# Kernel tuning notes

Measured on AMD Instinct MI355X. Metric: run time of the kernel, lower is better.

The kernel has to match this reference:

```python
import jax, jax.numpy as jnp
import numpy as np

N = 100000   # nodes
E = 1200000  # edges
D = 64       # input_features == hidden_features
L = 3        # num_layers
EPS = 1e-5   # BatchNorm1d eps
SLOPE = 0.2  # LeakyReLU negative slope


def setup_inputs() -> dict:
    key = jax.random.key(0)
    k_x, k_e, k_w = jax.random.split(key, 3)
    x = jax.random.normal(k_x, (N, D), dtype=jnp.float32)
    edge_index = jax.random.randint(k_e, (2, E), 0, N, dtype=jnp.int32)
    # Glorot-ish linear weights per layer, stacked [L, D, D]; bias zeros.
    Ws = jax.random.normal(k_w, (L, D, D), dtype=jnp.float32) / np.float32(np.sqrt(D))
    bs = jnp.zeros((L, D), dtype=jnp.float32)
    # BatchNorm affine params (training-mode batch statistics are used).
    gammas = jnp.ones((L, D), dtype=jnp.float32)
    betas = jnp.zeros((L, D), dtype=jnp.float32)
    return {"x": x, "edge_index": edge_index, "Ws": Ws, "bs": bs,
            "gammas": gammas, "betas": betas}


def reference(x, edge_index, Ws, bs, gammas, betas):
    src, dst = edge_index[0], edge_index[1]
    # GCN symmetric normalization with self-loops: deg = in-degree + 1
    deg = jax.ops.segment_sum(jnp.ones((E,), x.dtype), dst, num_segments=N) + 1.0
    dinv = jax.lax.rsqrt(deg)
    enorm = (dinv[src] * dinv[dst])[:, None]  # [E,1] edge norm
    snorm = (dinv * dinv)[:, None]            # [N,1] self-loop norm
    for l in range(L):
        xw = x @ Ws[l]                                        # [N,D]
        agg = (jax.ops.segment_sum(xw[src] * enorm, dst, num_segments=N)
               + xw * snorm + bs[l])                          # GCNConv output
        h = jnp.where(agg > 0, agg, SLOPE * agg)              # LeakyReLU(0.2)
        mu = h.mean(axis=0)
        var = h.var(axis=0)                                   # biased var (PyTorch BN)
        x = gammas[l] * (h - mu) * jax.lax.rsqrt(var + EPS) + betas[l]
    return x
```

## Files before the change

kernel.cpp:

```cpp
#include <hip/hip_runtime.h>

#define D 64
#define SLOPE 0.2f
#define BN_EPS 1e-5f
#define BSHIFT 9
#define CHUNK 7168

static __device__ __forceinline__ unsigned pk_bf16(float fx, float fy) {
    unsigned bx = __float_as_uint(fx);
    unsigned by = __float_as_uint(fy);
    bx = (bx + 0x7fffu + ((bx >> 16) & 1u)) >> 16;
    by = (by + 0x7fffu + ((by >> 16) & 1u)) & 0xffff0000u;
    return bx | by;
}
static __device__ __forceinline__ float bf_lo(unsigned u) { return __uint_as_float(u << 16); }
static __device__ __forceinline__ float bf_hi(unsigned u) { return __uint_as_float(u & 0xffff0000u); }

__global__ __launch_bounds__(256) void k_hist(const int* __restrict__ dst,
                                              int* __restrict__ bcnt, int E, int NB) {
    __shared__ int hist[256];
    for (int i = threadIdx.x; i < NB; i += 256) hist[i] = 0;
    __syncthreads();
    for (int e = blockIdx.x * 256 + threadIdx.x; e < E; e += gridDim.x * 256)
        atomicAdd(&hist[dst[e] >> BSHIFT], 1);
    __syncthreads();
    for (int i = threadIdx.x; i < NB; i += 256)
        if (hist[i]) atomicAdd(&bcnt[i], hist[i]);
}

__global__ __launch_bounds__(256) void k_bscan(const int* __restrict__ bcnt,
                                               int* __restrict__ bbase, int* __restrict__ pcur,
                                               int* __restrict__ rp, int NB, int E, int N) {
    __shared__ int l[256];
    const int t = threadIdx.x;
    const int v = (t < NB) ? bcnt[t] : 0;
    l[t] = v;
    __syncthreads();
    for (int off = 1; off < 256; off <<= 1) {
        int x = l[t];
        if (t >= off) x += l[t - off];
        __syncthreads();
        l[t] = x;
        __syncthreads();
    }
    if (t < NB) {
        const int excl = l[t] - v;
        bbase[t] = excl;
        pcur[t]  = excl;
    }
    if (t == 0) { bbase[NB] = E; rp[N] = E; }
}

__global__ __launch_bounds__(256) void k_part(const int* __restrict__ src,
                                              const int* __restrict__ dst,
                                              int* __restrict__ pcur,
                                              uint2* __restrict__ arena,
                                              int E, int NB, int nchunks) {
    __shared__ uint2 stage[CHUNK];
    __shared__ int hist[256], lofs[256], gbase[256];

    for (int chunk = blockIdx.x; chunk < nchunks; chunk += gridDim.x) {
        const int e0 = chunk * CHUNK;
        const int cn = min(CHUNK, E - e0);

        for (int i = threadIdx.x; i < NB; i += 256) hist[i] = 0;
        __syncthreads();
        for (int i = threadIdx.x; i < cn; i += 256)
            atomicAdd(&hist[dst[e0 + i] >> BSHIFT], 1);
        __syncthreads();

        {
            const int t = threadIdx.x;
            const int v = (t < NB) ? hist[t] : 0;
            l_scan:
            lofs[t] = v;
            __syncthreads();
            for (int off = 1; off < 256; off <<= 1) {
                int x = lofs[t];
                if (t >= off) x += lofs[t - off];
                __syncthreads();
                lofs[t] = x;
                __syncthreads();
            }
            const int excl = lofs[t] - v;
            __syncthreads();
            lofs[t] = excl;
            if (t < NB && v > 0) gbase[t] = atomicAdd(&pcur[t], v);
            __syncthreads();
        }

        for (int i = threadIdx.x; i < cn; i += 256) {
            const int d = dst[e0 + i];
            const int s = src[e0 + i];
            const int b = d >> BSHIFT;
            const int p = atomicAdd(&lofs[b], 1);
            stage[p] = make_uint2((unsigned)s, (unsigned)d);
        }
        __syncthreads();

        for (int i = threadIdx.x; i < cn; i += 256) {
            const uint2 u = stage[i];
            const int b = (int)(u.y >> BSHIFT);
            const int startb = lofs[b] - hist[b];
            arena[gbase[b] + (i - startb)] = u;
        }
        __syncthreads();
    }
}

__global__ __launch_bounds__(512) void k_build(const uint2* __restrict__ arena,
                                               const int* __restrict__ bbase,
                                               int* __restrict__ rp, int* __restrict__ colbuf,
                                               float* __restrict__ dinv, int N) {
    const int b = blockIdx.x;
    const int nbase = b << BSHIFT;
    const int nlocal = min(1 << BSHIFT, N - nbase);
    const int abeg = bbase[b];
    const int aend = bbase[b + 1];
    __shared__ int ncnt[512], sc[512], lcur[512];
    const int t = threadIdx.x;

    ncnt[t] = 0;
    __syncthreads();
    for (int i = abeg + t; i < aend; i += 512)
        atomicAdd(&ncnt[(int)(arena[i].y) - nbase], 1);
    __syncthreads();

    const int v = ncnt[t];
    sc[t] = v;
    __syncthreads();
    for (int off = 1; off < 512; off <<= 1) {
        int x = sc[t];
        if (t >= off) x += sc[t - off];
        __syncthreads();
        sc[t] = x;
        __syncthreads();
    }
    const int excl = sc[t] - v;
    lcur[t] = excl;
    if (t < nlocal) {
        rp[nbase + t]   = abeg + excl;
        dinv[nbase + t] = rsqrtf((float)v + 1.0f);
    }
    __syncthreads();

    for (int i = abeg + t; i < aend; i += 512) {
        const uint2 u = arena[i];
        const int ln = (int)u.y - nbase;
        const int p = atomicAdd(&lcur[ln], 1);
        colbuf[abeg + p] = (int)u.x;
    }
}

__global__ void k_prep(const float* __restrict__ W, const float* __restrict__ stats,
                       const float* __restrict__ gamma, const float* __restrict__ beta,
                       float* __restrict__ Wp, float* __restrict__ bvec,
                       float invN, int affine) {
    __shared__ float scs[D], shs[D];
    const int t = threadIdx.x;
    if (t < D) {
        float sc = 1.0f, sh = 0.0f;
        if (affine) {
            const float mu  = stats[t] * invN;
            const float var = stats[D + t] * invN - mu * mu;
            sc = gamma[t] * rsqrtf(var + BN_EPS);
            sh = beta[t] - mu * sc;
        }
        scs[t] = sc; shs[t] = sh;
    }
    __syncthreads();
    for (int i = t; i < D * D; i += blockDim.x)
        Wp[i] = scs[i >> 6] * W[i];
    if (t < D) {
        float s = 0.0f;
#pragma unroll
        for (int k = 0; k < D; ++k) s += shs[k] * W[k * D + t];
        bvec[t] = s;
    }
}

__global__ __launch_bounds__(256) void k_gemm(const float* __restrict__ x,
                                              const float* __restrict__ Wp,
                                              const float* __restrict__ bvec,
                                              const float* __restrict__ dinv,
                                              unsigned* __restrict__ ybf, int N) {
    const int lane = threadIdx.x & 63;
    const int wib  = threadIdx.x >> 6;
    float Wreg[D];
#pragma unroll
    for (int k = 0; k < D; ++k) Wreg[k] = Wp[k * D + lane];
    const float bv = bvec[lane];
    const int stride = gridDim.x * 4;

    for (int row = __builtin_amdgcn_readfirstlane(blockIdx.x * 4 + wib); row < N; row += stride) {
        const float4* xr = (const float4*)(x + (size_t)row * D);
        float acc = 0.0f;
#pragma unroll
        for (int k4 = 0; k4 < 16; ++k4) {
            const float4 xv = xr[k4];
            acc = fmaf(xv.x, Wreg[4 * k4 + 0], acc);
            acc = fmaf(xv.y, Wreg[4 * k4 + 1], acc);
            acc = fmaf(xv.z, Wreg[4 * k4 + 2], acc);
            acc = fmaf(xv.w, Wreg[4 * k4 + 3], acc);
        }
        const float r  = (acc + bv) * dinv[row];
        const float rn = __shfl_down(r, 1, 64);
        if (!(lane & 1))
            ybf[(size_t)row * 32 + (lane >> 1)] = pk_bf16(r, rn);
    }
}

__global__ __launch_bounds__(256) void k_pull(const int* __restrict__ rp,
                                              const int* __restrict__ colbuf,
                                              const uint2* __restrict__ ybf2,
                                              const float* __restrict__ dinv,
                                              const float* __restrict__ bvecin,
                                              float* __restrict__ h,
                                              float* __restrict__ stats, int N) {
    const int lane = threadIdx.x & 63;
    const int sl   = lane & 15;
    const int qw   = lane >> 4;
    const int wib  = threadIdx.x >> 6;
    const float4 bb = *(const float4*)&bvecin[4 * sl];
    const float* bp = &bb.x;
    float s1[4] = {0.f, 0.f, 0.f, 0.f}, s2[4] = {0.f, 0.f, 0.f, 0.f};

    const int wid = blockIdx.x * 4 + wib;
    const int wstride = gridDim.x * 4;

    for (int n0 = wid * 2; n0 < N; n0 += wstride * 2) {
        const int n1 = n0 + 1;
        const bool has1 = n1 < N;
        const int2 r01 = *(const int2*)&rp[n0];
        const int start = r01.x;
        const int mid   = r01.y;
        const int end   = has1 ? rp[n0 + 2] : r01.y;

        float a[4][4], ba[4][4];
#pragma unroll
        for (int c = 0; c < 4; ++c)
#pragma unroll
            for (int f = 0; f < 4; ++f) { a[c][f] = 0.f; ba[c][f] = 0.f; }

        if (qw == 0) {
            const uint2 u = ybf2[(size_t)n0 * 16 + sl];
            a[0][0] += bf_lo(u.x); a[0][1] += bf_hi(u.x);
            a[0][2] += bf_lo(u.y); a[0][3] += bf_hi(u.y);
        } else if (qw == 1 && has1) {
            const uint2 u = ybf2[(size_t)n1 * 16 + sl];
            const float f0 = bf_lo(u.x), f1 = bf_hi(u.x), f2 = bf_lo(u.y), f3 = bf_hi(u.y);
            a[0][0] += f0; a[0][1] += f1; a[0][2] += f2; a[0][3] += f3;
            ba[0][0] += f0; ba[0][1] += f1; ba[0][2] += f2; ba[0][3] += f3;
        }

        for (int j = start; j < end; j += 64) {
            const int rem = end - j;
            const int cn  = rem < 64 ? rem : 64;
            const int ci  = (lane < cn) ? colbuf[j + lane] : 0;
            for (int s = 0; 16 * s < cn; ++s) {
#pragma unroll
                for (int c = 0; c < 4; ++c) {
                    const int e   = 16 * s + 4 * c + qw;
                    const int idx = __shfl(ci, e, 64);
                    uint2 u = ybf2[(size_t)idx * 16 + sl];
                    const bool val = e < cn;
                    const bool is1 = (j + e) >= mid;
                    u.x = val ? u.x : 0u;
                    u.y = val ? u.y : 0u;
                    const float f0 = bf_lo(u.x), f1 = bf_hi(u.x);
                    const float f2 = bf_lo(u.y), f3 = bf_hi(u.y);
                    a[c][0] += f0; a[c][1] += f1; a[c][2] += f2; a[c][3] += f3;
                    ba[c][0] += is1 ? f0 : 0.f;
                    ba[c][1] += is1 ? f1 : 0.f;
                    ba[c][2] += is1 ? f2 : 0.f;
                    ba[c][3] += is1 ? f3 : 0.f;
                }
            }
        }

        float vA[4], vB[4];
#pragma unroll
        for (int f = 0; f < 4; ++f) {
            vA[f] = (a[0][f] + a[1][f]) + (a[2][f] + a[3][f]);
            vA[f] += __shfl_xor(vA[f], 16, 64);
            vA[f] += __shfl_xor(vA[f], 32, 64);
            vB[f] = (ba[0][f] + ba[1][f]) + (ba[2][f] + ba[3][f]);
            vB[f] += __shfl_xor(vB[f], 16, 64);
            vB[f] += __shfl_xor(vB[f], 32, 64);
        }

        if (qw == 0) {
            const float di = dinv[n0];
            float4 hv; float* hp = &hv.x;
#pragma unroll
            for (int f = 0; f < 4; ++f) {
                float t = fmaf(di, vA[f] - vB[f], bp[f]);
                t = t > 0.f ? t : SLOPE * t;
                hp[f] = t; s1[f] += t; s2[f] += t * t;
            }
            *(float4*)&h[(size_t)n0 * D + 4 * sl] = hv;
        } else if (qw == 1 && has1) {
            const float di = dinv[n1];
            float4 hv; float* hp = &hv.x;
#pragma unroll
            for (int f = 0; f < 4; ++f) {
                float t = fmaf(di, vB[f], bp[f]);
                t = t > 0.f ? t : SLOPE * t;
                hp[f] = t; s1[f] += t; s2[f] += t * t;
            }
            *(float4*)&h[(size_t)n1 * D + 4 * sl] = hv;
        }
    }

    __shared__ float s1d[8][16][4], s2d[8][16][4];
    if (qw < 2) {
#pragma unroll
        for (int f = 0; f < 4; ++f) {
            s1d[wib * 2 + qw][sl][f] = s1[f];
            s2d[wib * 2 + qw][sl][f] = s2[f];
        }
    }
    __syncthreads();
    const int tid = threadIdx.x;
    if (tid < 64) {
        const int ssl = tid >> 2, f = tid & 3;
        float A = 0.f, B = 0.f;
#pragma unroll
        for (int g = 0; g < 8; ++g) { A += s1d[g][ssl][f]; B += s2d[g][ssl][f]; }
        atomicAdd(&stats[tid], A);
        atomicAdd(&stats[64 + tid], B);
    }
}

__global__ void k_normalize(const float* __restrict__ h, const float* __restrict__ stats,
                            const float* __restrict__ gamma, const float* __restrict__ beta,
                            float* __restrict__ out, float invN, int total) {
    const int col = threadIdx.x & 63;
    const float mu  = stats[col] * invN;
    const float var = stats[64 + col] * invN - mu * mu;
    const float sc  = gamma[col] * rsqrtf(var + BN_EPS);
    const float sh  = beta[col] - mu * sc;
    for (int i = blockIdx.x * blockDim.x + threadIdx.x; i < total; i += gridDim.x * blockDim.x)
        out[i] = fmaf(sc, h[i], sh);
}

extern "C" void kernel_launch(void* const* d_in, const int* in_sizes, int n_in,
                              void* d_out, int out_size, void* d_ws, size_t ws_size,
                              hipStream_t stream) {
    const float* x0     = (const float*)d_in[0];
    const int*   ei     = (const int*)d_in[1];
    const float* Ws     = (const float*)d_in[2];
    const float* bs     = (const float*)d_in[3];
    const float* gammas = (const float*)d_in[4];
    const float* betas  = (const float*)d_in[5];

    const int N = in_sizes[0] / D;
    const int E = in_sizes[1] / 2;
    const int L = in_sizes[2] / (D * D);
    const int NB = (N + (1 << BSHIFT) - 1) >> BSHIFT;
    const int nchunks = (E + CHUNK - 1) / CHUNK;

    const int* srcp = ei;
    const int* dstp = ei + E;

    char* wsb = (char*)d_ws;
    size_t o = 0;
    auto alloc = [&](size_t elems) { size_t r = o; o += (elems + 255) & ~(size_t)255; return r; };
    const size_t o_bcnt  = alloc(256);
    const size_t o_stats = alloc((size_t)L * 128);
    const size_t zero_end = o;
    const size_t o_bbase = alloc(257);
    const size_t o_pcur  = alloc(256);
    const size_t o_rp    = alloc((size_t)N + 1);
    const size_t o_dinv  = alloc((size_t)N);
    const size_t o_arena = alloc((size_t)E * 2);
    const size_t o_col   = alloc((size_t)E);
    const size_t o_wp    = alloc((size_t)D * D);
    const size_t o_bvec  = alloc((size_t)D);
    const size_t o_y     = alloc((size_t)N * 32);
    const size_t o_h     = alloc((size_t)N * D);

    int*      bcnt  = (int*)(wsb + o_bcnt * 4);
    float*    stats = (float*)(wsb + o_stats * 4);
    int*      bbase = (int*)(wsb + o_bbase * 4);
    int*      pcur  = (int*)(wsb + o_pcur * 4);
    int*      rp    = (int*)(wsb + o_rp * 4);
    float*    dinv  = (float*)(wsb + o_dinv * 4);
    uint2*    arena = (uint2*)(wsb + o_arena * 4);
    int*      col   = (int*)(wsb + o_col * 4);
    float*    Wp    = (float*)(wsb + o_wp * 4);
    float*    bvec  = (float*)(wsb + o_bvec * 4);
    unsigned* ybf   = (unsigned*)(wsb + o_y * 4);
    float*    h     = (float*)(wsb + o_h * 4);
    float*    out   = (float*)d_out;

    hipMemsetAsync(d_ws, 0, zero_end * 4, stream);

    k_hist<<<512, 256, 0, stream>>>(dstp, bcnt, E, NB);
    k_bscan<<<1, 256, 0, stream>>>(bcnt, bbase, pcur, rp, NB, E, N);
    k_part<<<nchunks, 256, 0, stream>>>(srcp, dstp, pcur, arena, E, NB, nchunks);
    k_build<<<NB, 512, 0, stream>>>(arena, bbase, rp, col, dinv, N);

    const float invN = 1.0f / (float)N;
    const float* xin = x0;
    for (int l = 0; l < L; ++l) {
        const float* Wl = Ws + (size_t)l * D * D;
        const float* bl = bs + (size_t)l * D;
        k_prep<<<1, 256, 0, stream>>>(Wl, stats + (size_t)(l ? l - 1 : 0) * 128,
                                      gammas + (size_t)(l ? l - 1 : 0) * D,
                                      betas + (size_t)(l ? l - 1 : 0) * D,
                                      Wp, bvec, invN, l > 0 ? 1 : 0);
        k_gemm<<<1024, 256, 0, stream>>>(xin, Wp, bvec, dinv, ybf, N);
        k_pull<<<2048, 256, 0, stream>>>(rp, col, (const uint2*)ybf, dinv, bl, h,
                                         stats + (size_t)l * 128, N);
        xin = h;
    }
    k_normalize<<<1024, 256, 0, stream>>>(h, stats + (size_t)(L - 1) * 128,
                                          gammas + (size_t)(L - 1) * D,
                                          betas + (size_t)(L - 1) * D, out, invN, N * D);
}
```

Baseline: 424.1 us.

## Pack CSR edges, pad rows to multiples of eight, fuse prep into gemm

Edges are packed into 32-bit words holding the local destination and the source, which halves arena traffic in the partition and build passes. CSR rows are padded to multiples of eight and filled with a dummy zero row, so the pull kernel can gather unconditionally with half-wave-per-node unrolled loads. The per-layer BN-folding prep kernel is merged into the GEMM, which saves a launch per layer. Normalization now uses float4 accesses. The packing caps sources below 2^23 and adds padding memory plus wasted gathers on the dummy row.

```diff
diff --git a/kernel.cpp b/kernel.cpp
--- a/kernel.cpp
+++ b/kernel.cpp
@@ -4,7 +4,8 @@
 #define SLOPE 0.2f
 #define BN_EPS 1e-5f
 #define BSHIFT 9
-#define CHUNK 7168
+#define BUCKET 512
+#define CHUNK 8192
 
 static __device__ __forceinline__ unsigned pk_bf16(float fx, float fy) {
     unsigned bx = __float_as_uint(fx);
@@ -17,20 +18,20 @@
 static __device__ __forceinline__ float bf_hi(unsigned u) { return __uint_as_float(u & 0xffff0000u); }
 
 __global__ __launch_bounds__(256) void k_hist(const int* __restrict__ dst,
-                                              int* __restrict__ bcnt, int E, int NB) {
+                                              int* __restrict__ bcnt, int E) {
     __shared__ int hist[256];
-    for (int i = threadIdx.x; i < NB; i += 256) hist[i] = 0;
+    hist[threadIdx.x] = 0;
     __syncthreads();
     for (int e = blockIdx.x * 256 + threadIdx.x; e < E; e += gridDim.x * 256)
         atomicAdd(&hist[dst[e] >> BSHIFT], 1);
     __syncthreads();
-    for (int i = threadIdx.x; i < NB; i += 256)
-        if (hist[i]) atomicAdd(&bcnt[i], hist[i]);
+    const int v = hist[threadIdx.x];
+    if (v) atomicAdd(&bcnt[threadIdx.x], v);
 }
 
 __global__ __launch_bounds__(256) void k_bscan(const int* __restrict__ bcnt,
                                                int* __restrict__ bbase, int* __restrict__ pcur,
-                                               int* __restrict__ rp, int NB, int E, int N) {
+                                               unsigned* __restrict__ ybf, int NB, int E, int N) {
     __shared__ int l[256];
     const int t = threadIdx.x;
     const int v = (t < NB) ? bcnt[t] : 0;
@@ -43,91 +44,79 @@
         l[t] = x;
         __syncthreads();
     }
-    if (t < NB) {
-        const int excl = l[t] - v;
-        bbase[t] = excl;
-        pcur[t]  = excl;
-    }
-    if (t == 0) { bbase[NB] = E; rp[N] = E; }
+    const int excl = l[t] - v;
+    if (t < NB) { bbase[t] = excl; pcur[t] = excl; }
+    if (t == 0) bbase[NB] = E;
+    if (t < 32) ybf[(size_t)N * 32 + t] = 0u;
 }
 
 __global__ __launch_bounds__(256) void k_part(const int* __restrict__ src,
                                               const int* __restrict__ dst,
                                               int* __restrict__ pcur,
-                                              uint2* __restrict__ arena,
-                                              int E, int NB, int nchunks) {
-    __shared__ uint2 stage[CHUNK];
+                                              unsigned* __restrict__ arena, int E) {
+    __shared__ unsigned stage[CHUNK];
+    __shared__ unsigned char bktb[CHUNK];
     __shared__ int hist[256], lofs[256], gbase[256];
-
-    for (int chunk = blockIdx.x; chunk < nchunks; chunk += gridDim.x) {
-        const int e0 = chunk * CHUNK;
-        const int cn = min(CHUNK, E - e0);
-
-        for (int i = threadIdx.x; i < NB; i += 256) hist[i] = 0;
-        __syncthreads();
-        for (int i = threadIdx.x; i < cn; i += 256)
-            atomicAdd(&hist[dst[e0 + i] >> BSHIFT], 1);
-        __syncthreads();
-
-        {
-            const int t = threadIdx.x;
-            const int v = (t < NB) ? hist[t] : 0;
-            l_scan:
-            lofs[t] = v;
-            __syncthreads();
-            for (int off = 1; off < 256; off <<= 1) {
-                int x = lofs[t];
-                if (t >= off) x += lofs[t - off];
-                __syncthreads();
-                lofs[t] = x;
-                __syncthreads();
-            }
-            const int excl = lofs[t] - v;
-            __syncthreads();
-            lofs[t] = excl;
-            if (t < NB && v > 0) gbase[t] = atomicAdd(&pcur[t], v);
-            __syncthreads();
-        }
-
-        for (int i = threadIdx.x; i < cn; i += 256) {
-            const int d = dst[e0 + i];
-            const int s = src[e0 + i];
-            const int b = d >> BSHIFT;
-            const int p = atomicAdd(&lofs[b], 1);
-            stage[p] = make_uint2((unsigned)s, (unsigned)d);
-        }
-        __syncthreads();
-
-        for (int i = threadIdx.x; i < cn; i += 256) {
-            const uint2 u = stage[i];
-            const int b = (int)(u.y >> BSHIFT);
-            const int startb = lofs[b] - hist[b];
-            arena[gbase[b] + (i - startb)] = u;
-        }
-        __syncthreads();
-    }
-}
-
-__global__ __launch_bounds__(512) void k_build(const uint2* __restrict__ arena,
+    const int t = threadIdx.x;
+    const int e0 = blockIdx.x * CHUNK;
+    const int cn = min(CHUNK, E - e0);
+
+    hist[t] = 0;
+    __syncthreads();
+    for (int i = t; i < cn; i += 256)
+        atomicAdd(&hist[dst[e0 + i] >> BSHIFT], 1);
+    __syncthreads();
+    const int v = hist[t];
+    lofs[t] = v;
+    __syncthreads();
+    for (int off = 1; off < 256; off <<= 1) {
+        int x = lofs[t];
+        if (t >= off) x += lofs[t - off];
+        __syncthreads();
+        lofs[t] = x;
+        __syncthreads();
+    }
+    const int excl = lofs[t] - v;
+    __syncthreads();
+    lofs[t] = excl;
+    if (v > 0) gbase[t] = atomicAdd(&pcur[t], v);
+    __syncthreads();
+    for (int i = t; i < cn; i += 256) {
+        const int dd = dst[e0 + i];
+        const int b  = dd >> BSHIFT;
+        const int p  = atomicAdd(&lofs[b], 1);
+        stage[p] = ((unsigned)(dd & (BUCKET - 1)) << 23) | (unsigned)src[e0 + i];
+        bktb[p]  = (unsigned char)b;
+    }
+    __syncthreads();
+    for (int i = t; i < cn; i += 256) {
+        const int b = bktb[i];
+        const int startb = lofs[b] - hist[b];
+        arena[gbase[b] + (i - startb)] = stage[i];
+    }
+}
+
+__global__ __launch_bounds__(512) void k_build(const unsigned* __restrict__ arena,
                                                const int* __restrict__ bbase,
-                                               int* __restrict__ rp, int* __restrict__ colbuf,
-                                               float* __restrict__ dinv, int N) {
-    const int b = blockIdx.x;
-    const int nbase = b << BSHIFT;
-    const int nlocal = min(1 << BSHIFT, N - nbase);
-    const int abeg = bbase[b];
-    const int aend = bbase[b + 1];
+                                               int* __restrict__ rp, int* __restrict__ pcnt,
+                                               int* __restrict__ colbuf, float* __restrict__ dinv,
+                                               int N) {
     __shared__ int ncnt[512], sc[512], lcur[512];
     const int t = threadIdx.x;
+    const int nbase  = blockIdx.x << BSHIFT;
+    const int nlocal = min(BUCKET, N - nbase);
+    const int abeg = bbase[blockIdx.x];
+    const int aend = bbase[blockIdx.x + 1];
+    const int pbase = abeg + 7 * nbase;
 
     ncnt[t] = 0;
     __syncthreads();
     for (int i = abeg + t; i < aend; i += 512)
-        atomicAdd(&ncnt[(int)(arena[i].y) - nbase], 1);
-    __syncthreads();
-
+        atomicAdd(&ncnt[arena[i] >> 23], 1);
+    __syncthreads();
     const int v = ncnt[t];
-    sc[t] = v;
+    const int p = (v + 7) & ~7;
+    sc[t] = p;
     __syncthreads();
     for (int off = 1; off < 512; off <<= 1) {
         int x = sc[t];
@@ -136,65 +125,59 @@
         sc[t] = x;
         __syncthreads();
     }
-    const int excl = sc[t] - v;
-    lcur[t] = excl;
+    const int excl = sc[t] - p;
+    lcur[t] = pbase + excl;
     if (t < nlocal) {
-        rp[nbase + t]   = abeg + excl;
+        rp[nbase + t]   = pbase + excl;
+        pcnt[nbase + t] = p;
         dinv[nbase + t] = rsqrtf((float)v + 1.0f);
     }
     __syncthreads();
-
     for (int i = abeg + t; i < aend; i += 512) {
-        const uint2 u = arena[i];
-        const int ln = (int)u.y - nbase;
-        const int p = atomicAdd(&lcur[ln], 1);
-        colbuf[abeg + p] = (int)u.x;
-    }
-}
-
-__global__ void k_prep(const float* __restrict__ W, const float* __restrict__ stats,
-                       const float* __restrict__ gamma, const float* __restrict__ beta,
-                       float* __restrict__ Wp, float* __restrict__ bvec,
-                       float invN, int affine) {
+        const unsigned u = arena[i];
+        const int pos = atomicAdd(&lcur[u >> 23], 1);
+        colbuf[pos] = (int)(u & 0x7FFFFFu);
+    }
+    if (t < nlocal)
+        for (int k = v; k < p; ++k) colbuf[pbase + excl + k] = N;
+}
+
+__global__ __launch_bounds__(256) void k_gemm(const float* __restrict__ x,
+                                              const float* __restrict__ W,
+                                              const float* __restrict__ stats,
+                                              const float* __restrict__ gamma,
+                                              const float* __restrict__ beta,
+                                              const float* __restrict__ dinv,
+                                              unsigned* __restrict__ ybf,
+                                              float invN, int affine, int N) {
     __shared__ float scs[D], shs[D];
-    const int t = threadIdx.x;
-    if (t < D) {
-        float sc = 1.0f, sh = 0.0f;
+    const int tid = threadIdx.x;
+    if (tid < D) {
+        float sc = 1.f, sh = 0.f;
         if (affine) {
-            const float mu  = stats[t] * invN;
-            const float var = stats[D + t] * invN - mu * mu;
-            sc = gamma[t] * rsqrtf(var + BN_EPS);
-            sh = beta[t] - mu * sc;
-        }
-        scs[t] = sc; shs[t] = sh;
-    }
-    __syncthreads();
-    for (int i = t; i < D * D; i += blockDim.x)
-        Wp[i] = scs[i >> 6] * W[i];
-    if (t < D) {
-        float s = 0.0f;
-#pragma unroll
-        for (int k = 0; k < D; ++k) s += shs[k] * W[k * D + t];
-        bvec[t] = s;
-    }
-}
-
-__global__ __launch_bounds__(256) void k_gemm(const float* __restrict__ x,
-                                              const float* __restrict__ Wp,
-                                              const float* __restrict__ bvec,
-                                              const float* __restrict__ dinv,
-                                              unsigned* __restrict__ ybf, int N) {
-    const int lane = threadIdx.x & 63;
-    const int wib  = threadIdx.x >> 6;
+            const float mu  = stats[tid] * invN;
+            const float var = stats[D + tid] * invN - mu * mu;
+            sc = gamma[tid] * rsqrtf(var + BN_EPS);
+            sh = beta[tid] - mu * sc;
+        }
+        scs[tid] = sc; shs[tid] = sh;
+    }
+    __syncthreads();
+
+    const int lane = tid & 63;
+    const int wib  = tid >> 6;
     float Wreg[D];
-#pragma unroll
-    for (int k = 0; k < D; ++k) Wreg[k] = Wp[k * D + lane];
-    const float bv = bvec[lane];
+    float bv = 0.f;
+#pragma unroll
+    for (int k = 0; k < D; ++k) {
+        const float w = W[k * D + lane];
+        Wreg[k] = scs[k] * w;
+        bv = fmaf(shs[k], w, bv);
+    }
     const int stride = gridDim.x * 4;
-
     for (int row = __builtin_amdgcn_readfirstlane(blockIdx.x * 4 + wib); row < N; row += stride) {
         const float4* xr = (const float4*)(x + (size_t)row * D);
-        float acc = 0.0f;
+        float acc = 0.f;
 #pragma unroll
         for (int k4 = 0; k4 < 16; ++k4) {
             const float4 xv = xr[k4];
@@ -211,137 +194,106 @@
 }
 
 __global__ __launch_bounds__(256) void k_pull(const int* __restrict__ rp,
+                                              const int* __restrict__ pcnt,
                                               const int* __restrict__ colbuf,
-                                              const uint2* __restrict__ ybf2,
+                                              const unsigned* __restrict__ ybf,
                                               const float* __restrict__ dinv,
-                                              const float* __restrict__ bvecin,
+                                              const float* __restrict__ b,
                                               float* __restrict__ h,
                                               float* __restrict__ stats, int N) {
-    const int lane = threadIdx.x & 63;
-    const int sl   = lane & 15;
-    const int qw   = lane >> 4;
-    const int wib  = threadIdx.x >> 6;
-    const float4 bb = *(const float4*)&bvecin[4 * sl];
-    const float* bp = &bb.x;
-    float s1[4] = {0.f, 0.f, 0.f, 0.f}, s2[4] = {0.f, 0.f, 0.f, 0.f};
-
-    const int wid = blockIdx.x * 4 + wib;
-    const int wstride = gridDim.x * 4;
-
-    for (int n0 = wid * 2; n0 < N; n0 += wstride * 2) {
-        const int n1 = n0 + 1;
-        const bool has1 = n1 < N;
-        const int2 r01 = *(const int2*)&rp[n0];
-        const int start = r01.x;
-        const int mid   = r01.y;
-        const int end   = has1 ? rp[n0 + 2] : r01.y;
-
-        float a[4][4], ba[4][4];
-#pragma unroll
-        for (int c = 0; c < 4; ++c)
-#pragma unroll
-            for (int f = 0; f < 4; ++f) { a[c][f] = 0.f; ba[c][f] = 0.f; }
-
-        if (qw == 0) {
-            const uint2 u = ybf2[(size_t)n0 * 16 + sl];
-            a[0][0] += bf_lo(u.x); a[0][1] += bf_hi(u.x);
-            a[0][2] += bf_lo(u.y); a[0][3] += bf_hi(u.y);
-        } else if (qw == 1 && has1) {
-            const uint2 u = ybf2[(size_t)n1 * 16 + sl];
-            const float f0 = bf_lo(u.x), f1 = bf_hi(u.x), f2 = bf_lo(u.y), f3 = bf_hi(u.y);
-            a[0][0] += f0; a[0][1] += f1; a[0][2] += f2; a[0][3] += f3;
-            ba[0][0] += f0; ba[0][1] += f1; ba[0][2] += f2; ba[0][3] += f3;
-        }
-
-        for (int j = start; j < end; j += 64) {
-            const int rem = end - j;
-            const int cn  = rem < 64 ? rem : 64;
-            const int ci  = (lane < cn) ? colbuf[j + lane] : 0;
-            for (int s = 0; 16 * s < cn; ++s) {
-#pragma unroll
-                for (int c = 0; c < 4; ++c) {
-                    const int e   = 16 * s + 4 * c + qw;
-                    const int idx = __shfl(ci, e, 64);
-                    uint2 u = ybf2[(size_t)idx * 16 + sl];
-                    const bool val = e < cn;
-                    const bool is1 = (j + e) >= mid;
-                    u.x = val ? u.x : 0u;
-                    u.y = val ? u.y : 0u;
-                    const float f0 = bf_lo(u.x), f1 = bf_hi(u.x);
-                    const float f2 = bf_lo(u.y), f3 = bf_hi(u.y);
-                    a[c][0] += f0; a[c][1] += f1; a[c][2] += f2; a[c][3] += f3;
-                    ba[c][0] += is1 ? f0 : 0.f;
-                    ba[c][1] += is1 ? f1 : 0.f;
-                    ba[c][2] += is1 ? f2 : 0.f;
-                    ba[c][3] += is1 ? f3 : 0.f;
+    const int tid  = threadIdx.x;
+    const int lane = tid & 63;
+    const int t32  = lane & 31;
+    const int hw   = lane >> 5;
+    const int wv   = tid >> 6;
+    const float b0 = b[2 * t32];
+    const float b1 = b[2 * t32 + 1];
+    float s1a = 0.f, s1b = 0.f, s2a = 0.f, s2b = 0.f;
+
+    const int gw = blockIdx.x * 4 + wv;
+    const int gstride = gridDim.x * 4;
+
+    for (int pr = gw; 2 * pr < N; pr += gstride) {
+        const int n  = 2 * pr + hw;
+        const bool vn = n < N;
+        const int st = vn ? rp[n]   : 0;
+        const int pd = vn ? pcnt[n] : 0;
+
+        float a[8][2];
+#pragma unroll
+        for (int c = 0; c < 8; ++c) { a[c][0] = 0.f; a[c][1] = 0.f; }
+        {
+            const unsigned u = vn ? ybf[(size_t)n * 32 + t32] : 0u;
+            a[0][0] = bf_lo(u); a[0][1] = bf_hi(u);
+        }
+        for (int w0 = 0; w0 < pd; w0 += 32) {
+            const int wn = min(pd - w0, 32);
+            const int ci = (t32 < wn) ? colbuf[st + w0 + t32] : 0;
+            for (int j0 = 0; j0 < wn; j0 += 8) {
+#pragma unroll
+                for (int jj = 0; jj < 8; ++jj) {
+                    const int idx = __shfl(ci, hw * 32 + j0 + jj, 64);
+                    const unsigned u = ybf[(size_t)idx * 32 + t32];
+                    a[jj][0] += bf_lo(u);
+                    a[jj][1] += bf_hi(u);
                 }
             }
         }
-
-        float vA[4], vB[4];
-#pragma unroll
-        for (int f = 0; f < 4; ++f) {
-            vA[f] = (a[0][f] + a[1][f]) + (a[2][f] + a[3][f]);
-            vA[f] += __shfl_xor(vA[f], 16, 64);
-            vA[f] += __shfl_xor(vA[f], 32, 64);
-            vB[f] = (ba[0][f] + ba[1][f]) + (ba[2][f] + ba[3][f]);
-            vB[f] += __shfl_xor(vB[f], 16, 64);
-            vB[f] += __shfl_xor(vB[f], 32, 64);
-        }
-
-        if (qw == 0) {
-            const float di = dinv[n0];
-            float4 hv; float* hp = &hv.x;
-#pragma unroll
-            for (int f = 0; f < 4; ++f) {
-                float t = fmaf(di, vA[f] - vB[f], bp[f]);
-                t = t > 0.f ? t : SLOPE * t;
-                hp[f] = t; s1[f] += t; s2[f] += t * t;
-            }
-            *(float4*)&h[(size_t)n0 * D + 4 * sl] = hv;
-        } else if (qw == 1 && has1) {
-            const float di = dinv[n1];
-            float4 hv; float* hp = &hv.x;
-#pragma unroll
-            for (int f = 0; f < 4; ++f) {
-                float t = fmaf(di, vB[f], bp[f]);
-                t = t > 0.f ? t : SLOPE * t;
-                hp[f] = t; s1[f] += t; s2[f] += t * t;
-            }
-            *(float4*)&h[(size_t)n1 * D + 4 * sl] = hv;
-        }
-    }
-
-    __shared__ float s1d[8][16][4], s2d[8][16][4];
-    if (qw < 2) {
-#pragma unroll
-        for (int f = 0; f < 4; ++f) {
-            s1d[wib * 2 + qw][sl][f] = s1[f];
-            s2d[wib * 2 + qw][sl][f] = s2[f];
-        }
-    }
-    __syncthreads();
-    const int tid = threadIdx.x;
+        const float v0 = ((a[0][0] + a[1][0]) + (a[2][0] + a[3][0])) +
+                         ((a[4][0] + a[5][0]) + (a[6][0] + a[7][0]));
+        const float v1 = ((a[0][1] + a[1][1]) + (a[2][1] + a[3][1])) +
+                         ((a[4][1] + a[5][1]) + (a[6][1] + a[7][1]));
+        if (vn) {
+            const float di = dinv[n];
+            float t0 = fmaf(di, v0, b0); t0 = t0 > 0.f ? t0 : SLOPE * t0;
+            float t1 = fmaf(di, v1, b1); t1 = t1 > 0.f ? t1 : SLOPE * t1;
+            *(float2*)&h[(size_t)n * D + 2 * t32] = make_float2(t0, t1);
+            s1a += t0; s2a += t0 * t0;
+            s1b += t1; s2b += t1 * t1;
+        }
+    }
+
+    __shared__ float l1[64], l2[64];
+    if (tid < 64) { l1[tid] = 0.f; l2[tid] = 0.f; }
+    __syncthreads();
+    atomicAdd(&l1[2 * t32],     s1a);
+    atomicAdd(&l1[2 * t32 + 1], s1b);
+    atomicAdd(&l2[2 * t32],     s2a);
+    atomicAdd(&l2[2 * t32 + 1], s2b);
+    __syncthreads();
     if (tid < 64) {
-        const int ssl = tid >> 2, f = tid & 3;
-        float A = 0.f, B = 0.f;
-#pragma unroll
-        for (int g = 0; g < 8; ++g) { A += s1d[g][ssl][f]; B += s2d[g][ssl][f]; }
-        atomicAdd(&stats[tid], A);
-        atomicAdd(&stats[64 + tid], B);
-    }
-}
-
-__global__ void k_normalize(const float* __restrict__ h, const float* __restrict__ stats,
-                            const float* __restrict__ gamma, const float* __restrict__ beta,
-                            float* __restrict__ out, float invN, int total) {
-    const int col = threadIdx.x & 63;
-    const float mu  = stats[col] * invN;
-    const float var = stats[64 + col] * invN - mu * mu;
-    const float sc  = gamma[col] * rsqrtf(var + BN_EPS);
-    const float sh  = beta[col] - mu * sc;
-    for (int i = blockIdx.x * blockDim.x + threadIdx.x; i < total; i += gridDim.x * blockDim.x)
-        out[i] = fmaf(sc, h[i], sh);
+        atomicAdd(&stats[tid],      l1[tid]);
+        atomicAdd(&stats[64 + tid], l2[tid]);
+    }
+}
+
+__global__ __launch_bounds__(256) void k_normalize(const float* __restrict__ h,
+                                                   const float* __restrict__ stats,
+                                                   const float* __restrict__ gamma,
+                                                   const float* __restrict__ beta,
+                                                   float* __restrict__ out,
+                                                   float invN, int total4) {
+    const int gt = blockIdx.x * 256 + threadIdx.x;
+    const int c0 = (gt * 4) & 63;
+    float sc[4], sh[4];
+#pragma unroll
+    for (int k = 0; k < 4; ++k) {
+        const int c = c0 + k;
+        const float mu  = stats[c] * invN;
+        const float var = stats[64 + c] * invN - mu * mu;
+        sc[k] = gamma[c] * rsqrtf(var + BN_EPS);
+        sh[k] = beta[c] - mu * sc[k];
+    }
+    const float4* h4 = (const float4*)h;
+    float4* o4 = (float4*)out;
+    for (int i = gt; i < total4; i += gridDim.x * 256) {
+        float4 v = h4[i];
+        v.x = fmaf(sc[0], v.x, sh[0]);
+        v.y = fmaf(sc[1], v.y, sh[1]);
+        v.z = fmaf(sc[2], v.z, sh[2]);
+        v.w = fmaf(sc[3], v.w, sh[3]);
+        o4[i] = v;
+    }
 }
 
 extern "C" void kernel_launch(void* const* d_in, const int* in_sizes, int n_in,
@@ -357,7 +309,7 @@
     const int N = in_sizes[0] / D;
     const int E = in_sizes[1] / 2;
     const int L = in_sizes[2] / (D * D);
-    const int NB = (N + (1 << BSHIFT) - 1) >> BSHIFT;
+    const int NB = (N + BUCKET - 1) >> BSHIFT;
     const int nchunks = (E + CHUNK - 1) / CHUNK;
 
     const int* srcp = ei;
@@ -371,13 +323,12 @@
     const size_t zero_end = o;
     const size_t o_bbase = alloc(257);
     const size_t o_pcur  = alloc(256);
-    const size_t o_rp    = alloc((size_t)N + 1);
+    const size_t o_rp    = alloc((size_t)N);
+    const size_t o_pcnt  = alloc((size_t)N);
     const size_t o_dinv  = alloc((size_t)N);
-    const size_t o_arena = alloc((size_t)E * 2);
-    const size_t o_col   = alloc((size_t)E);
-    const size_t o_wp    = alloc((size_t)D * D);
-    const size_t o_bvec  = alloc((size_t)D);
-    const size_t o_y     = alloc((size_t)N * 32);
+    const size_t o_arena = alloc((size_t)E);
+    const size_t o_col   = alloc((size_t)E + 7 * (size_t)N + 64);
+    const size_t o_y     = alloc(((size_t)N + 1) * 32);
     const size_t o_h     = alloc((size_t)N * D);
 
     int*      bcnt  = (int*)(wsb + o_bcnt * 4);
@@ -385,37 +336,35 @@
     int*      bbase = (int*)(wsb + o_bbase * 4);
     int*      pcur  = (int*)(wsb + o_pcur * 4);
     int*      rp    = (int*)(wsb + o_rp * 4);
+    int*      pcnt  = (int*)(wsb + o_pcnt * 4);
     float*    dinv  = (float*)(wsb + o_dinv * 4);
-    uint2*    arena = (uint2*)(wsb + o_arena * 4);
+    unsigned* arena = (unsigned*)(wsb + o_arena * 4);
     int*      col   = (int*)(wsb + o_col * 4);
-    float*    Wp    = (float*)(wsb + o_wp * 4);
-    float*    bvec  = (float*)(wsb + o_bvec * 4);
     unsigned* ybf   = (unsigned*)(wsb + o_y * 4);
     float*    h     = (float*)(wsb + o_h * 4);
     float*    out   = (float*)d_out;
 
     hipMemsetAsync(d_ws, 0, zero_end * 4, stream);
 
-    k_hist<<<512, 256, 0, stream>>>(dstp, bcnt, E, NB);
-    k_bscan<<<1, 256, 0, stream>>>(bcnt, bbase, pcur, rp, NB, E, N);
-    k_part<<<nchunks, 256, 0, stream>>>(srcp, dstp, pcur, arena, E, NB, nchunks);
-    k_build<<<NB, 512, 0, stream>>>(arena, bbase, rp, col, dinv, N);
+    k_hist <<<512, 256, 0, stream>>>(dstp, bcnt, E);
+    k_bscan<<<1,   256, 0, stream>>>(bcnt, bbase, pcur, ybf, NB, E, N);
+    k_part <<<nchunks, 256, 0, stream>>>(srcp, dstp, pcur, arena, E);
+    k_build<<<NB,  512, 0, stream>>>(arena, bbase, rp, pcnt, col, dinv, N);
 
     const float invN = 1.0f / (float)N;
     const float* xin = x0;
     for (int l = 0; l < L; ++l) {
-        const float* Wl = Ws + (size_t)l * D * D;
-        const float* bl = bs + (size_t)l * D;
-        k_prep<<<1, 256, 0, stream>>>(Wl, stats + (size_t)(l ? l - 1 : 0) * 128,
-                                      gammas + (size_t)(l ? l - 1 : 0) * D,
-                                      betas + (size_t)(l ? l - 1 : 0) * D,
-                                      Wp, bvec, invN, l > 0 ? 1 : 0);
-        k_gemm<<<1024, 256, 0, stream>>>(xin, Wp, bvec, dinv, ybf, N);
-        k_pull<<<2048, 256, 0, stream>>>(rp, col, (const uint2*)ybf, dinv, bl, h,
-                                         stats + (size_t)l * 128, N);
+        const int pl = l ? l - 1 : 0;
+        k_gemm<<<1024, 256, 0, stream>>>(xin, Ws + (size_t)l * D * D,
+                                         stats + (size_t)pl * 128,
+                                         gammas + (size_t)pl * D, betas + (size_t)pl * D,
+                                         dinv, ybf, invN, l > 0 ? 1 : 0, N);
+        k_pull<<<2048, 256, 0, stream>>>(rp, pcnt, col, ybf, dinv, bs + (size_t)l * D,
+                                         h, stats + (size_t)l * 128, N);
         xin = h;
     }
     k_normalize<<<1024, 256, 0, stream>>>(h, stats + (size_t)(L - 1) * 128,
                                           gammas + (size_t)(L - 1) * D,
-                                          betas + (size_t)(L - 1) * D, out, invN, N * D);
-}
+                                          betas + (size_t)(L - 1) * D,
+                                          out, invN, N * D / 4);
+}
```

Measured after the change: 407.3 us. -3.9%, faster.
